# Kernel optimization log

Hardware: AMD Instinct MI355X
Metric: run time of the kernel (lower is better)

The kernel has to match this reference:

```python
import jax, jax.numpy as jnp
import numpy as np

H = 128        # num_hidden
NIN = 384      # num_in
FF = 4 * H
SCALE = 30.0
EPS = 1e-5


def _gelu(x):
    return jax.nn.gelu(x, approximate=False)


def _layernorm(x, g, b):
    mu = jnp.mean(x, axis=-1, keepdims=True)
    var = jnp.var(x, axis=-1, keepdims=True)
    return (x - mu) * jax.lax.rsqrt(var + EPS) * g + b


def setup_inputs() -> dict:
    key = jax.random.key(0)
    ks = jax.random.split(key, 12)
    B, N, K = 4, 2048, 48
    s = lambda fan_in: 1.0 / np.sqrt(fan_in)
    inp = {
        "h_V": jax.random.normal(ks[0], (B, N, H), jnp.float32),
        "h_E": jax.random.normal(ks[1], (B, N, K, NIN), jnp.float32),
        "mask_V": jnp.ones((B, N), jnp.float32),
        "mask_attend": jnp.ones((B, N, K), jnp.float32),
        "W1_w": jax.random.uniform(ks[2], (H + NIN, H), jnp.float32, -s(H + NIN), s(H + NIN)),
        "W1_b": jnp.zeros((H,), jnp.float32),
        "W2_w": jax.random.uniform(ks[3], (H, H), jnp.float32, -s(H), s(H)),
        "W2_b": jnp.zeros((H,), jnp.float32),
        "W3_w": jax.random.uniform(ks[4], (H, H), jnp.float32, -s(H), s(H)),
        "W3_b": jnp.zeros((H,), jnp.float32),
        "Win_w": jax.random.uniform(ks[5], (H, FF), jnp.float32, -s(H), s(H)),
        "Win_b": jnp.zeros((FF,), jnp.float32),
        "Wout_w": jax.random.uniform(ks[6], (FF, H), jnp.float32, -s(FF), s(FF)),
        "Wout_b": jnp.zeros((H,), jnp.float32),
        "ln1_g": jnp.ones((H,), jnp.float32),
        "ln1_b": jnp.zeros((H,), jnp.float32),
        "ln2_g": jnp.ones((H,), jnp.float32),
        "ln2_b": jnp.zeros((H,), jnp.float32),
    }
    return inp


def reference(h_V, h_E, mask_V, mask_attend,
              W1_w, W1_b, W2_w, W2_b, W3_w, W3_b,
              Win_w, Win_b, Wout_w, Wout_b,
              ln1_g, ln1_b, ln2_g, ln2_b):
    B, N, K, _ = h_E.shape
    # expand node feats over K neighbors and concat with edge feats -> [B,N,K,H+NIN]
    h_V_expand = jnp.broadcast_to(h_V[:, :, None, :], (B, N, K, h_V.shape[-1]))
    h_EV = jnp.concatenate([h_V_expand, h_E], axis=-1)
    # edge MLP: 3 linears, 2 GELUs
    h_message = _gelu(h_EV @ W1_w + W1_b)
    h_message = _gelu(h_message @ W2_w + W2_b)
    h_message = h_message @ W3_w + W3_b
    h_message = mask_attend[..., None] * h_message
    dh = jnp.sum(h_message, axis=-2) / SCALE  # [B,N,H]
    h = _layernorm(h_V + dh, ln1_g, ln1_b)
    # position-wise FFN
    dh = _gelu(h @ Win_w + Win_b) @ Wout_w + Wout_b
    h = _layernorm(h + dh, ln2_g, ln2_b)
    h = mask_V[..., None] * h
    return h
```

## Files before the change

kernel.cpp:

```cpp
#include <hip/hip_runtime.h>
#include <hip/hip_bf16.h>

#define Hh    128
#define NINc  384
#define KN    48
#define FFd   512
#define NNODE 8192

typedef __attribute__((ext_vector_type(8))) short short8v;
typedef __attribute__((ext_vector_type(4))) float f32x4;

__device__ __forceinline__ short f2bf1(float f){
  union { __hip_bfloat16 h; short s; } c; c.h = __float2bfloat16(f);
  return c.s;
}
__device__ __forceinline__ unsigned pk_bf16(float lo, float hi){
  union { __hip_bfloat162 h; unsigned u; } c;
  c.h = __float22bfloat162_rn(make_float2(lo, hi));
  return c.u;
}

__device__ __forceinline__ float gelu_f(float x){
  float t = 0.7978845608028654f * x * (1.0f + 0.044715f * x * x);
  float e = __expf(2.0f * t);
  return x * (1.0f - 1.0f / (e + 1.0f));
}

__device__ __forceinline__ void bar_lds(){
  asm volatile("s_waitcnt lgkmcnt(0)\n\ts_barrier" ::: "memory");
}

__global__ void prep_weights(const float* __restrict__ W1, const float* __restrict__ W2,
                             const float* __restrict__ W3, const float* __restrict__ Win,
                             const float* __restrict__ Wout,
                             short* __restrict__ w1vT, short* __restrict__ w1p,
                             short* __restrict__ w2p,  short* __restrict__ w3p,
                             short* __restrict__ winT, short* __restrict__ woutT)
{
  int i = blockIdx.x * 256 + threadIdx.x;
  if (i < 16384){ int n = i / 128, k = i % 128; w1vT[i] = f2bf1(W1[k*128 + n]); return; }
  i -= 16384;
  if (i < 49152){
    int n = i / 6144, r = i % 6144;
    int ks = r / 512, r2 = r % 512;
    int lane = r2 / 8, j = r2 % 8;
    int qq = lane >> 4, arow = lane & 15;
    w1p[i] = f2bf1(W1[(128 + ks*32 + qq*8 + j)*128 + n*16 + arow]); return;
  }
  i -= 49152;
  if (i < 16384){
    int n = i / 2048, r = i % 2048;
    int ks = r / 512, r2 = r % 512;
    int lane = r2 / 8, j = r2 % 8;
    int qq = lane >> 4, arow = lane & 15;
    w2p[i] = f2bf1(W2[(ks*32 + qq*8 + j)*128 + n*16 + arow]); return;
  }
  i -= 16384;
  if (i < 16384){
    int n = i / 2048, r = i % 2048;
    int ks = r / 512, r2 = r % 512;
    int lane = r2 / 8, j = r2 % 8;
    int qq = lane >> 4, arow = lane & 15;
    w3p[i] = f2bf1(W3[(ks*32 + qq*8 + j)*128 + n*16 + arow]); return;
  }
  i -= 16384;
  if (i < 65536){ int n = i / 128, k = i % 128; winT[i] = f2bf1(Win[k*512 + n]); return; }
  i -= 65536;
  if (i < 65536){ int n = i / 512, k = i % 512; woutT[i] = f2bf1(Wout[k*128 + n]); return; }
}

__global__ __launch_bounds__(256,2) void np_kernel(
    const float* __restrict__ hV, const short* __restrict__ w1vT,
    const float* __restrict__ b1, float* __restrict__ npart)
{
  const int row0 = blockIdx.x * 64;
  const int tid = threadIdx.x, lane = tid & 63, wv = tid >> 6;
  __shared__ __attribute__((aligned(16))) short Xs[64][Hh + 8];

  const float4* src = (const float4*)(hV + (size_t)row0 * Hh);
  #pragma unroll
  for (int j = 0; j < 8; ++j){
    int idx = tid + 256*j;
    int r = idx >> 5, c4 = idx & 31;
    float4 v = src[idx];
    *(uint2*)&Xs[r][c4*4] = make_uint2(pk_bf16(v.x,v.y), pk_bf16(v.z,v.w));
  }
  __syncthreads();

  const int arow = lane & 15, kgrp = (lane >> 4) * 8;
  const int col0 = wv * 32, ccol = lane & 15, crow0 = (lane >> 4) * 4;

  f32x4 acc[4][2];
  #pragma unroll
  for (int m = 0; m < 4; ++m) for (int n = 0; n < 2; ++n) acc[m][n] = (f32x4){0.f,0.f,0.f,0.f};

  const short8v* Bw = (const short8v*)w1vT;
  #pragma unroll
  for (int ks = 0; ks < 4; ++ks){
    int kb = ks*32 + kgrp;
    short8v b0 = Bw[(col0 + arow)*16      + (kb >> 3)];
    short8v b1f = Bw[(col0 + 16 + arow)*16 + (kb >> 3)];
    #pragma unroll
    for (int m = 0; m < 4; ++m){
      short8v a = *(const short8v*)&Xs[m*16 + arow][kb];
      acc[m][0] = __builtin_amdgcn_mfma_f32_16x16x32_bf16(a, b0,  acc[m][0], 0,0,0);
      acc[m][1] = __builtin_amdgcn_mfma_f32_16x16x32_bf16(a, b1f, acc[m][1], 0,0,0);
    }
  }
  #pragma unroll
  for (int m = 0; m < 4; ++m) for (int n = 0; n < 2; ++n){
    int colg = col0 + n*16 + ccol;
    float bb = b1[colg];
    #pragma unroll
    for (int r = 0; r < 4; ++r)
      npart[(size_t)(row0 + m*16 + crow0 + r)*Hh + colg] = acc[m][n][r] + bb;
  }
}

__global__ __launch_bounds__(256,3) void edge_kernel(
    const float* __restrict__ hE, const float* __restrict__ hV,
    const float* __restrict__ maskA, const float* __restrict__ npart,
    const short* __restrict__ w1p, const short* __restrict__ w2p,
    const short* __restrict__ w3p,
    const float* __restrict__ b2, const float* __restrict__ b3,
    float* __restrict__ out)
{
  const int node = blockIdx.x;
  const int tid = threadIdx.x, lane = tid & 63, wv = tid >> 6;
  const int e = lane & 15, q = lane >> 4, kgrp = q * 8;
  const int n0 = wv * 32;

  __shared__ __attribute__((aligned(16))) short Et[KN][NINc + 8];
  __shared__ __attribute__((aligned(16))) short M1[KN][136];
  short (*M2)[136] = (short (*)[136])&Et[0][0];

  {
    const float4* src = (const float4*)(hE + (size_t)node * (KN*NINc));
    #pragma unroll
    for (int h = 0; h < 2; ++h){
      float4 pf[9];
      #pragma unroll
      for (int j = 0; j < 9; ++j) pf[j] = src[tid + 256*(9*h + j)];
      #pragma unroll
      for (int j = 0; j < 9; ++j){
        int idx = tid + 256*(9*h + j);
        int r = idx / 96, c4 = idx - r*96;
        *(uint2*)&Et[r][c4*4] = make_uint2(pk_bf16(pf[j].x, pf[j].y),
                                           pk_bf16(pf[j].z, pf[j].w));
      }
    }
  }

  const float4 npv0 = *(const float4*)(npart + (size_t)node*Hh + n0 + 4*q);
  const float4 npv1 = *(const float4*)(npart + (size_t)node*Hh + n0 + 16 + 4*q);
  const float4 b2v0 = *(const float4*)(b2 + n0 + 4*q);
  const float4 b2v1 = *(const float4*)(b2 + n0 + 16 + 4*q);
  const float4 b3v0 = *(const float4*)(b3 + n0 + 4*q);
  const float4 b3v1 = *(const float4*)(b3 + n0 + 16 + 4*q);
  const float4 hvv0 = *(const float4*)(hV + (size_t)node*Hh + n0 + 4*q);
  const float4 hvv1 = *(const float4*)(hV + (size_t)node*Hh + n0 + 16 + 4*q);
  const float mk0 = maskA[node*KN + e];
  const float mk1 = maskA[node*KN + 16 + e];
  const float mk2 = maskA[node*KN + 32 + e];

  __syncthreads();

  const f32x4 Z = (f32x4){0.f,0.f,0.f,0.f};

  {
    f32x4 a00=Z, a10=Z, a20=Z, a01=Z, a11=Z, a21=Z;
    const short8v* B1 = (const short8v*)w1p;
    #pragma unroll
    for (int ks = 0; ks < 12; ++ks){
      short8v f0 = B1[((2*wv  )*12 + ks)*64 + lane];
      short8v f1 = B1[((2*wv+1)*12 + ks)*64 + lane];
      int kb = ks*32 + kgrp;
      short8v t0 = *(const short8v*)&Et[e][kb];
      short8v t1 = *(const short8v*)&Et[16 + e][kb];
      short8v t2 = *(const short8v*)&Et[32 + e][kb];
      a00 = __builtin_amdgcn_mfma_f32_16x16x32_bf16(f0, t0, a00, 0,0,0);
      a10 = __builtin_amdgcn_mfma_f32_16x16x32_bf16(f0, t1, a10, 0,0,0);
      a20 = __builtin_amdgcn_mfma_f32_16x16x32_bf16(f0, t2, a20, 0,0,0);
      a01 = __builtin_amdgcn_mfma_f32_16x16x32_bf16(f1, t0, a01, 0,0,0);
      a11 = __builtin_amdgcn_mfma_f32_16x16x32_bf16(f1, t1, a11, 0,0,0);
      a21 = __builtin_amdgcn_mfma_f32_16x16x32_bf16(f1, t2, a21, 0,0,0);
    }
    #define WR_M(DST, ACC, ET, COLB, BV)  { short4 s;                 \
      s.x = f2bf1(gelu_f(ACC[0] + BV.x));                             \
      s.y = f2bf1(gelu_f(ACC[1] + BV.y));                             \
      s.z = f2bf1(gelu_f(ACC[2] + BV.z));                             \
      s.w = f2bf1(gelu_f(ACC[3] + BV.w));                             \
      *(short4*)&DST[16*ET + e][COLB + 4*q] = s; }
    WR_M(M1, a00, 0, n0,      npv0)  WR_M(M1, a10, 1, n0,      npv0)
    WR_M(M1, a20, 2, n0,      npv0)  WR_M(M1, a01, 0, n0 + 16, npv1)
    WR_M(M1, a11, 1, n0 + 16, npv1)  WR_M(M1, a21, 2, n0 + 16, npv1)
  }
  bar_lds();

  {
    f32x4 c00=Z, c10=Z, c20=Z, c01=Z, c11=Z, c21=Z;
    const short8v* B2f = (const short8v*)w2p;
    #pragma unroll
    for (int ks = 0; ks < 4; ++ks){
      short8v f0 = B2f[((2*wv  )*4 + ks)*64 + lane];
      short8v f1 = B2f[((2*wv+1)*4 + ks)*64 + lane];
      int kb = ks*32 + kgrp;
      short8v t0 = *(const short8v*)&M1[e][kb];
      short8v t1 = *(const short8v*)&M1[16 + e][kb];
      short8v t2 = *(const short8v*)&M1[32 + e][kb];
      c00 = __builtin_amdgcn_mfma_f32_16x16x32_bf16(f0, t0, c00, 0,0,0);
      c10 = __builtin_amdgcn_mfma_f32_16x16x32_bf16(f0, t1, c10, 0,0,0);
      c20 = __builtin_amdgcn_mfma_f32_16x16x32_bf16(f0, t2, c20, 0,0,0);
      c01 = __builtin_amdgcn_mfma_f32_16x16x32_bf16(f1, t0, c01, 0,0,0);
      c11 = __builtin_amdgcn_mfma_f32_16x16x32_bf16(f1, t1, c11, 0,0,0);
      c21 = __builtin_amdgcn_mfma_f32_16x16x32_bf16(f1, t2, c21, 0,0,0);
    }
    WR_M(M2, c00, 0, n0,      b2v0)  WR_M(M2, c10, 1, n0,      b2v0)
    WR_M(M2, c20, 2, n0,      b2v0)  WR_M(M2, c01, 0, n0 + 16, b2v1)
    WR_M(M2, c11, 1, n0 + 16, b2v1)  WR_M(M2, c21, 2, n0 + 16, b2v1)
  }
  bar_lds();

  {
    f32x4 d00=Z, d10=Z, d20=Z, d01=Z, d11=Z, d21=Z;
    const short8v* B3f = (const short8v*)w3p;
    #pragma unroll
    for (int ks = 0; ks < 4; ++ks){
      short8v f0 = B3f[((2*wv  )*4 + ks)*64 + lane];
      short8v f1 = B3f[((2*wv+1)*4 + ks)*64 + lane];
      int kb = ks*32 + kgrp;
      short8v t0 = *(const short8v*)&M2[e][kb];
      short8v t1 = *(const short8v*)&M2[16 + e][kb];
      short8v t2 = *(const short8v*)&M2[32 + e][kb];
      d00 = __builtin_amdgcn_mfma_f32_16x16x32_bf16(f0, t0, d00, 0,0,0);
      d10 = __builtin_amdgcn_mfma_f32_16x16x32_bf16(f0, t1, d10, 0,0,0);
      d20 = __builtin_amdgcn_mfma_f32_16x16x32_bf16(f0, t2, d20, 0,0,0);
      d01 = __builtin_amdgcn_mfma_f32_16x16x32_bf16(f1, t0, d01, 0,0,0);
      d11 = __builtin_amdgcn_mfma_f32_16x16x32_bf16(f1, t1, d11, 0,0,0);
      d21 = __builtin_amdgcn_mfma_f32_16x16x32_bf16(f1, t2, d21, 0,0,0);
    }
    f32x4 v0, v1;
    #pragma unroll
    for (int r = 0; r < 4; ++r){
      v0[r] = (d00[r] + b3v0[r])*mk0 + (d10[r] + b3v0[r])*mk1 + (d20[r] + b3v0[r])*mk2;
      v1[r] = (d01[r] + b3v1[r])*mk0 + (d11[r] + b3v1[r])*mk1 + (d21[r] + b3v1[r])*mk2;
    }
    #pragma unroll
    for (int s = 1; s <= 8; s <<= 1){
      #pragma unroll
      for (int r = 0; r < 4; ++r){
        v0[r] += __shfl_xor(v0[r], s);
        v1[r] += __shfl_xor(v1[r], s);
      }
    }
    if (e == 0){
      float4 o0, o1;
      o0.x = hvv0.x + v0[0]*(1.0f/30.0f); o0.y = hvv0.y + v0[1]*(1.0f/30.0f);
      o0.z = hvv0.z + v0[2]*(1.0f/30.0f); o0.w = hvv0.w + v0[3]*(1.0f/30.0f);
      o1.x = hvv1.x + v1[0]*(1.0f/30.0f); o1.y = hvv1.y + v1[1]*(1.0f/30.0f);
      o1.z = hvv1.z + v1[2]*(1.0f/30.0f); o1.w = hvv1.w + v1[3]*(1.0f/30.0f);
      *(float4*)(out + (size_t)node*Hh + n0 + 4*q)      = o0;
      *(float4*)(out + (size_t)node*Hh + n0 + 16 + 4*q) = o1;
    }
  }
  #undef WR_M
}

__global__ __launch_bounds__(256,2) void ffn_kernel(
    const float* __restrict__ ln1g, const float* __restrict__ ln1b,
    const short* __restrict__ winT, const float* __restrict__ bin,
    const short* __restrict__ woutT, const float* __restrict__ bout,
    const float* __restrict__ ln2g, const float* __restrict__ ln2b,
    const float* __restrict__ maskV, float* __restrict__ io)
{
  const int row0 = blockIdx.x * 32;
  const int tid = threadIdx.x, lane = tid & 63, wv = tid >> 6;
  __shared__ __attribute__((aligned(16))) short Xs[32][Hh + 8];
  __shared__ __attribute__((aligned(16))) float Rs[32][Hh + 4];
  __shared__ __attribute__((aligned(16))) short Hs[32][FFd + 8];

  const int arow = lane & 15, kgrp = (lane >> 4) * 8;
  const int ccol = lane & 15, crow0 = (lane >> 4) * 4;

  {
    int r = tid >> 3, cb = (tid & 7) * 16;
    const float4* xp = (const float4*)(io + (size_t)(row0 + r)*Hh + cb);
    float xv[16];
    #pragma unroll
    for (int j = 0; j < 4; ++j){
      float4 v = xp[j];
      xv[j*4+0]=v.x; xv[j*4+1]=v.y; xv[j*4+2]=v.z; xv[j*4+3]=v.w;
    }
    float sum = 0.f, sq = 0.f;
    #pragma unroll
    for (int j = 0; j < 16; ++j){ sum += xv[j]; sq += xv[j]*xv[j]; }
    #pragma unroll
    for (int d = 1; d < 8; d <<= 1){ sum += __shfl_xor(sum, d); sq += __shfl_xor(sq, d); }
    float mu = sum * (1.0f/128.0f);
    float var = sq * (1.0f/128.0f) - mu*mu;
    float rstd = rsqrtf(var + 1e-5f);
    #pragma unroll
    for (int j = 0; j < 16; ++j){
      int c = cb + j;
      float xn = (xv[j] - mu) * rstd * ln1g[c] + ln1b[c];
      Xs[r][c] = f2bf1(xn);
      Rs[r][c] = xn;
    }
  }
  __syncthreads();

  {
    f32x4 acc[2][8];
    #pragma unroll
    for (int m = 0; m < 2; ++m) for (int n = 0; n < 8; ++n) acc[m][n] = (f32x4){0.f,0.f,0.f,0.f};
    const short8v* Bw = (const short8v*)winT;
    #pragma unroll
    for (int ks = 0; ks < 4; ++ks){
      int kb = ks*32 + kgrp;
      short8v a0 = *(const short8v*)&Xs[arow][kb];
      short8v a1 = *(const short8v*)&Xs[16 + arow][kb];
      #pragma unroll
      for (int n = 0; n < 8; ++n){
        short8v b = Bw[(wv*128 + n*16 + arow)*16 + (kb >> 3)];
        acc[0][n] = __builtin_amdgcn_mfma_f32_16x16x32_bf16(a0,b,acc[0][n],0,0,0);
        acc[1][n] = __builtin_amdgcn_mfma_f32_16x16x32_bf16(a1,b,acc[1][n],0,0,0);
      }
    }
    #pragma unroll
    for (int m = 0; m < 2; ++m) for (int n = 0; n < 8; ++n){
      int colg = wv*128 + n*16 + ccol;
      float bb = bin[colg];
      #pragma unroll
      for (int r = 0; r < 4; ++r)
        Hs[m*16 + crow0 + r][colg] = f2bf1(gelu_f(acc[m][n][r] + bb));
    }
  }
  __syncthreads();

  {
    f32x4 acc[2][2];
    #pragma unroll
    for (int m = 0; m < 2; ++m) for (int n = 0; n < 2; ++n) acc[m][n] = (f32x4){0.f,0.f,0.f,0.f};
    const short8v* Bw = (const short8v*)woutT;
    #pragma unroll
    for (int ks = 0; ks < 16; ++ks){
      int kb = ks*32 + kgrp;
      short8v a0 = *(const short8v*)&Hs[arow][kb];
      short8v a1 = *(const short8v*)&Hs[16 + arow][kb];
      short8v b0 = Bw[(wv*32 + arow)*64      + (kb >> 3)];
      short8v b1f = Bw[(wv*32 + 16 + arow)*64 + (kb >> 3)];
      acc[0][0] = __builtin_amdgcn_mfma_f32_16x16x32_bf16(a0,b0, acc[0][0],0,0,0);
      acc[1][0] = __builtin_amdgcn_mfma_f32_16x16x32_bf16(a1,b0, acc[1][0],0,0,0);
      acc[0][1] = __builtin_amdgcn_mfma_f32_16x16x32_bf16(a0,b1f,acc[0][1],0,0,0);
      acc[1][1] = __builtin_amdgcn_mfma_f32_16x16x32_bf16(a1,b1f,acc[1][1],0,0,0);
    }
    #pragma unroll
    for (int m = 0; m < 2; ++m) for (int n = 0; n < 2; ++n){
      int colg = wv*32 + n*16 + ccol;
      float bb = bout[colg];
      #pragma unroll
      for (int r = 0; r < 4; ++r){
        int rr = m*16 + crow0 + r;
        Rs[rr][colg] = Rs[rr][colg] + acc[m][n][r] + bb;
      }
    }
  }
  __syncthreads();

  {
    int r = tid >> 3, cb = (tid & 7) * 16;
    float xv[16];
    #pragma unroll
    for (int j = 0; j < 16; ++j) xv[j] = Rs[r][cb + j];
    float sum = 0.f, sq = 0.f;
    #pragma unroll
    for (int j = 0; j < 16; ++j){ sum += xv[j]; sq += xv[j]*xv[j]; }
    #pragma unroll
    for (int d = 1; d < 8; d <<= 1){ sum += __shfl_xor(sum, d); sq += __shfl_xor(sq, d); }
    float mu = sum * (1.0f/128.0f);
    float var = sq * (1.0f/128.0f) - mu*mu;
    float rstd = rsqrtf(var + 1e-5f);
    float mv = maskV[row0 + r];
    float* op = io + (size_t)(row0 + r)*Hh + cb;
    #pragma unroll
    for (int j = 0; j < 4; ++j){
      float4 o;
      o.x = ((xv[j*4+0] - mu)*rstd*ln2g[cb+j*4+0] + ln2b[cb+j*4+0]) * mv;
      o.y = ((xv[j*4+1] - mu)*rstd*ln2g[cb+j*4+1] + ln2b[cb+j*4+1]) * mv;
      o.z = ((xv[j*4+2] - mu)*rstd*ln2g[cb+j*4+2] + ln2b[cb+j*4+2]) * mv;
      o.w = ((xv[j*4+3] - mu)*rstd*ln2g[cb+j*4+3] + ln2b[cb+j*4+3]) * mv;
      ((float4*)op)[j] = o;
    }
  }
}

extern "C" void kernel_launch(void* const* d_in, const int* in_sizes, int n_in,
                              void* d_out, int out_size, void* d_ws, size_t ws_size,
                              hipStream_t stream)
{
  const float* hV    = (const float*)d_in[0];
  const float* hE    = (const float*)d_in[1];
  const float* maskV = (const float*)d_in[2];
  const float* maskA = (const float*)d_in[3];
  const float* W1w   = (const float*)d_in[4];
  const float* W1b   = (const float*)d_in[5];
  const float* W2w   = (const float*)d_in[6];
  const float* W2b   = (const float*)d_in[7];
  const float* W3w   = (const float*)d_in[8];
  const float* W3b   = (const float*)d_in[9];
  const float* Winw  = (const float*)d_in[10];
  const float* Winb  = (const float*)d_in[11];
  const float* Woutw = (const float*)d_in[12];
  const float* Woutb = (const float*)d_in[13];
  const float* l1g   = (const float*)d_in[14];
  const float* l1b   = (const float*)d_in[15];
  const float* l2g   = (const float*)d_in[16];
  const float* l2b   = (const float*)d_in[17];

  char* ws = (char*)d_ws;
  size_t off = 0;
  float* npart = (float*)(ws + off); off += (size_t)NNODE * Hh * 4;
  short* w1vT  = (short*)(ws + off); off += 16384*2;
  short* w1p   = (short*)(ws + off); off += 49152*2;
  short* w2p   = (short*)(ws + off); off += 16384*2;
  short* w3p   = (short*)(ws + off); off += 16384*2;
  short* winT  = (short*)(ws + off); off += 65536*2;
  short* woutT = (short*)(ws + off); off += 65536*2;
  if (ws_size < off) return;

  prep_weights<<<896, 256, 0, stream>>>(W1w, W2w, W3w, Winw, Woutw,
                                        w1vT, w1p, w2p, w3p, winT, woutT);
  np_kernel<<<NNODE/64, 256, 0, stream>>>(hV, w1vT, W1b, npart);
  edge_kernel<<<NNODE, 256, 0, stream>>>(hE, hV, maskA, npart,
                                         w1p, w2p, w3p, W2b, W3b, (float*)d_out);
  ffn_kernel<<<NNODE/32, 256, 0, stream>>>(l1g, l1b, winT, Winb, woutT, Woutb,
                                           l2g, l2b, maskV, (float*)d_out);
}
```

Baseline: 212.9 us.

## Stream edge features directly from global into MFMA operands, drop LDS staging

After: 365.8 us. 71.8% more time.

```diff
diff --git a/kernel.cpp b/kernel.cpp
--- a/kernel.cpp
+++ b/kernel.cpp
@@ -19,6 +19,12 @@
   c.h = __float22bfloat162_rn(make_float2(lo, hi));
   return c.u;
 }
+__device__ __forceinline__ short8v pack8(float4 a, float4 b){
+  union { short8v s; unsigned u[4]; } r;
+  r.u[0] = pk_bf16(a.x, a.y); r.u[1] = pk_bf16(a.z, a.w);
+  r.u[2] = pk_bf16(b.x, b.y); r.u[3] = pk_bf16(b.z, b.w);
+  return r.s;
+}
 
 __device__ __forceinline__ float gelu_f(float x){
   float t = 0.7978845608028654f * x * (1.0f + 0.044715f * x * x);
@@ -28,6 +34,13 @@
 
 __device__ __forceinline__ void bar_lds(){
   asm volatile("s_waitcnt lgkmcnt(0)\n\ts_barrier" ::: "memory");
+}
+
+__device__ __forceinline__ short* ldsAddr(short* base, int row, int colShort){
+  int raw  = colShort * 2;
+  int slot = raw >> 4, off = raw & 15;
+  int pslot = (slot & 8) | ((slot ^ row) & 7);
+  return (short*)((char*)base + row*256 + pslot*16 + off);
 }
 
 __global__ void prep_weights(const float* __restrict__ W1, const float* __restrict__ W2,
@@ -117,7 +130,7 @@
   }
 }
 
-__global__ __launch_bounds__(256,3) void edge_kernel(
+__global__ __launch_bounds__(256,4) void edge_kernel(
     const float* __restrict__ hE, const float* __restrict__ hV,
     const float* __restrict__ maskA, const float* __restrict__ npart,
     const short* __restrict__ w1p, const short* __restrict__ w2p,
@@ -127,29 +140,11 @@
 {
   const int node = blockIdx.x;
   const int tid = threadIdx.x, lane = tid & 63, wv = tid >> 6;
-  const int e = lane & 15, q = lane >> 4, kgrp = q * 8;
+  const int e = lane & 15, q = lane >> 4;
   const int n0 = wv * 32;
 
-  __shared__ __attribute__((aligned(16))) short Et[KN][NINc + 8];
-  __shared__ __attribute__((aligned(16))) short M1[KN][136];
-  short (*M2)[136] = (short (*)[136])&Et[0][0];
-
-  {
-    const float4* src = (const float4*)(hE + (size_t)node * (KN*NINc));
-    #pragma unroll
-    for (int h = 0; h < 2; ++h){
-      float4 pf[9];
-      #pragma unroll
-      for (int j = 0; j < 9; ++j) pf[j] = src[tid + 256*(9*h + j)];
-      #pragma unroll
-      for (int j = 0; j < 9; ++j){
-        int idx = tid + 256*(9*h + j);
-        int r = idx / 96, c4 = idx - r*96;
-        *(uint2*)&Et[r][c4*4] = make_uint2(pk_bf16(pf[j].x, pf[j].y),
-                                           pk_bf16(pf[j].z, pf[j].w));
-      }
-    }
-  }
+  __shared__ __attribute__((aligned(16))) short M1[KN * 128];
+  __shared__ __attribute__((aligned(16))) short M2[KN * 128];
 
   const float4 npv0 = *(const float4*)(npart + (size_t)node*Hh + n0 + 4*q);
   const float4 npv1 = *(const float4*)(npart + (size_t)node*Hh + n0 + 16 + 4*q);
@@ -163,9 +158,18 @@
   const float mk1 = maskA[node*KN + 16 + e];
   const float mk2 = maskA[node*KN + 32 + e];
 
-  __syncthreads();
-
   const f32x4 Z = (f32x4){0.f,0.f,0.f,0.f};
+  const float* eb = hE + (size_t)node * (KN*NINc);
+  const float* er0 = eb + (size_t)e        * NINc + q*8;
+  const float* er1 = eb + (size_t)(16 + e) * NINc + q*8;
+  const float* er2 = eb + (size_t)(32 + e) * NINc + q*8;
+
+  #define WR_M(DST, ACC, ET, COLB, BV)  { short4 s;                 \
+    s.x = f2bf1(gelu_f(ACC[0] + BV.x));                             \
+    s.y = f2bf1(gelu_f(ACC[1] + BV.y));                             \
+    s.z = f2bf1(gelu_f(ACC[2] + BV.z));                             \
+    s.w = f2bf1(gelu_f(ACC[3] + BV.w));                             \
+    *(short4*)ldsAddr(DST, 16*ET + e, COLB + 4*q) = s; }
 
   {
     f32x4 a00=Z, a10=Z, a20=Z, a01=Z, a11=Z, a21=Z;
@@ -174,10 +178,15 @@
     for (int ks = 0; ks < 12; ++ks){
       short8v f0 = B1[((2*wv  )*12 + ks)*64 + lane];
       short8v f1 = B1[((2*wv+1)*12 + ks)*64 + lane];
-      int kb = ks*32 + kgrp;
-      short8v t0 = *(const short8v*)&Et[e][kb];
-      short8v t1 = *(const short8v*)&Et[16 + e][kb];
-      short8v t2 = *(const short8v*)&Et[32 + e][kb];
+      float4 x0a = *(const float4*)(er0 + ks*32);
+      float4 x0b = *(const float4*)(er0 + ks*32 + 4);
+      float4 x1a = *(const float4*)(er1 + ks*32);
+      float4 x1b = *(const float4*)(er1 + ks*32 + 4);
+      float4 x2a = *(const float4*)(er2 + ks*32);
+      float4 x2b = *(const float4*)(er2 + ks*32 + 4);
+      short8v t0 = pack8(x0a, x0b);
+      short8v t1 = pack8(x1a, x1b);
+      short8v t2 = pack8(x2a, x2b);
       a00 = __builtin_amdgcn_mfma_f32_16x16x32_bf16(f0, t0, a00, 0,0,0);
       a10 = __builtin_amdgcn_mfma_f32_16x16x32_bf16(f0, t1, a10, 0,0,0);
       a20 = __builtin_amdgcn_mfma_f32_16x16x32_bf16(f0, t2, a20, 0,0,0);
@@ -185,12 +194,6 @@
       a11 = __builtin_amdgcn_mfma_f32_16x16x32_bf16(f1, t1, a11, 0,0,0);
       a21 = __builtin_amdgcn_mfma_f32_16x16x32_bf16(f1, t2, a21, 0,0,0);
     }
-    #define WR_M(DST, ACC, ET, COLB, BV)  { short4 s;                 \
-      s.x = f2bf1(gelu_f(ACC[0] + BV.x));                             \
-      s.y = f2bf1(gelu_f(ACC[1] + BV.y));                             \
-      s.z = f2bf1(gelu_f(ACC[2] + BV.z));                             \
-      s.w = f2bf1(gelu_f(ACC[3] + BV.w));                             \
-      *(short4*)&DST[16*ET + e][COLB + 4*q] = s; }
     WR_M(M1, a00, 0, n0,      npv0)  WR_M(M1, a10, 1, n0,      npv0)
     WR_M(M1, a20, 2, n0,      npv0)  WR_M(M1, a01, 0, n0 + 16, npv1)
     WR_M(M1, a11, 1, n0 + 16, npv1)  WR_M(M1, a21, 2, n0 + 16, npv1)
@@ -204,10 +207,10 @@
     for (int ks = 0; ks < 4; ++ks){
       short8v f0 = B2f[((2*wv  )*4 + ks)*64 + lane];
       short8v f1 = B2f[((2*wv+1)*4 + ks)*64 + lane];
-      int kb = ks*32 + kgrp;
-      short8v t0 = *(const short8v*)&M1[e][kb];
-      short8v t1 = *(const short8v*)&M1[16 + e][kb];
-      short8v t2 = *(const short8v*)&M1[32 + e][kb];
+      int kc = ks*32 + q*8;
+      short8v t0 = *(const short8v*)ldsAddr(M1, e,      kc);
+      short8v t1 = *(const short8v*)ldsAddr(M1, 16 + e, kc);
+      short8v t2 = *(const short8v*)ldsAddr(M1, 32 + e, kc);
       c00 = __builtin_amdgcn_mfma_f32_16x16x32_bf16(f0, t0, c00, 0,0,0);
       c10 = __builtin_amdgcn_mfma_f32_16x16x32_bf16(f0, t1, c10, 0,0,0);
       c20 = __builtin_amdgcn_mfma_f32_16x16x32_bf16(f0, t2, c20, 0,0,0);
@@ -228,10 +231,10 @@
     for (int ks = 0; ks < 4; ++ks){
       short8v f0 = B3f[((2*wv  )*4 + ks)*64 + lane];
       short8v f1 = B3f[((2*wv+1)*4 + ks)*64 + lane];
-      int kb = ks*32 + kgrp;
-      short8v t0 = *(const short8v*)&M2[e][kb];
-      short8v t1 = *(const short8v*)&M2[16 + e][kb];
-      short8v t2 = *(const short8v*)&M2[32 + e][kb];
+      int kc = ks*32 + q*8;
+      short8v t0 = *(const short8v*)ldsAddr(M2, e,      kc);
+      short8v t1 = *(const short8v*)ldsAddr(M2, 16 + e, kc);
+      short8v t2 = *(const short8v*)ldsAddr(M2, 32 + e, kc);
       d00 = __builtin_amdgcn_mfma_f32_16x16x32_bf16(f0, t0, d00, 0,0,0);
       d10 = __builtin_amdgcn_mfma_f32_16x16x32_bf16(f0, t1, d10, 0,0,0);
       d20 = __builtin_amdgcn_mfma_f32_16x16x32_bf16(f0, t2, d20, 0,0,0);
```

## Split each node's neighbors across two blocks and add combine kernel

Applied to the files above, without the earlier changes.

Result: slower. 241.4 us (+13.4%).

```diff
diff --git a/kernel.cpp b/kernel.cpp
--- a/kernel.cpp
+++ b/kernel.cpp
@@ -117,37 +117,46 @@
   }
 }
 
-__global__ __launch_bounds__(256,3) void edge_kernel(
-    const float* __restrict__ hE, const float* __restrict__ hV,
+__global__ __launch_bounds__(256,4) void edge_kernel(
+    const float* __restrict__ hE,
     const float* __restrict__ maskA, const float* __restrict__ npart,
     const short* __restrict__ w1p, const short* __restrict__ w2p,
     const short* __restrict__ w3p,
     const float* __restrict__ b2, const float* __restrict__ b3,
-    float* __restrict__ out)
-{
-  const int node = blockIdx.x;
+    float* __restrict__ pbuf)
+{
+  const int bid  = blockIdx.x;
+  const int node = bid >> 1, half = bid & 1;
   const int tid = threadIdx.x, lane = tid & 63, wv = tid >> 6;
-  const int e = lane & 15, q = lane >> 4, kgrp = q * 8;
+  const int e = lane & 15, q = lane >> 4;
   const int n0 = wv * 32;
 
-  __shared__ __attribute__((aligned(16))) short Et[KN][NINc + 8];
-  __shared__ __attribute__((aligned(16))) short M1[KN][136];
+  __shared__ __attribute__((aligned(16))) short Et[32][NINc + 8];
+  __shared__ __attribute__((aligned(16))) short M1[32][136];
   short (*M2)[136] = (short (*)[136])&Et[0][0];
 
   {
-    const float4* src = (const float4*)(hE + (size_t)node * (KN*NINc));
-    #pragma unroll
-    for (int h = 0; h < 2; ++h){
-      float4 pf[9];
-      #pragma unroll
-      for (int j = 0; j < 9; ++j) pf[j] = src[tid + 256*(9*h + j)];
-      #pragma unroll
-      for (int j = 0; j < 9; ++j){
-        int idx = tid + 256*(9*h + j);
-        int r = idx / 96, c4 = idx - r*96;
-        *(uint2*)&Et[r][c4*4] = make_uint2(pk_bf16(pf[j].x, pf[j].y),
-                                           pk_bf16(pf[j].z, pf[j].w));
-      }
+    unsigned* zp = (unsigned*)&Et[24][0];
+    #pragma unroll
+    for (int z = 0; z < 7; ++z) zp[tid + 256*z] = 0;
+    if (tid < 1568 - 1792 + 256) {}
+  }
+  {
+    unsigned* zp = (unsigned*)&Et[24][0];
+    for (int z = tid; z < 1568; z += 256) zp[z] = 0;
+  }
+
+  {
+    const float4* src = (const float4*)(hE + ((size_t)node*KN + half*24) * NINc);
+    float4 pf[9];
+    #pragma unroll
+    for (int j = 0; j < 9; ++j) pf[j] = src[tid + 256*j];
+    #pragma unroll
+    for (int j = 0; j < 9; ++j){
+      int idx = tid + 256*j;
+      int r = idx / 96, c4 = idx - r*96;
+      *(uint2*)&Et[r][c4*4] = make_uint2(pk_bf16(pf[j].x, pf[j].y),
+                                         pk_bf16(pf[j].z, pf[j].w));
     }
   }
 
@@ -157,93 +166,80 @@
   const float4 b2v1 = *(const float4*)(b2 + n0 + 16 + 4*q);
   const float4 b3v0 = *(const float4*)(b3 + n0 + 4*q);
   const float4 b3v1 = *(const float4*)(b3 + n0 + 16 + 4*q);
-  const float4 hvv0 = *(const float4*)(hV + (size_t)node*Hh + n0 + 4*q);
-  const float4 hvv1 = *(const float4*)(hV + (size_t)node*Hh + n0 + 16 + 4*q);
-  const float mk0 = maskA[node*KN + e];
-  const float mk1 = maskA[node*KN + 16 + e];
-  const float mk2 = maskA[node*KN + 32 + e];
+  const float mk0 = maskA[node*KN + half*24 + e];
+  const float mk1 = (e < 8) ? maskA[node*KN + half*24 + 16 + e] : 0.f;
 
   __syncthreads();
 
   const f32x4 Z = (f32x4){0.f,0.f,0.f,0.f};
 
-  {
-    f32x4 a00=Z, a10=Z, a20=Z, a01=Z, a11=Z, a21=Z;
+  #define WR_M(DST, ACC, ET, COLB, BV)  { short4 s;                 \
+    s.x = f2bf1(gelu_f(ACC[0] + BV.x));                             \
+    s.y = f2bf1(gelu_f(ACC[1] + BV.y));                             \
+    s.z = f2bf1(gelu_f(ACC[2] + BV.z));                             \
+    s.w = f2bf1(gelu_f(ACC[3] + BV.w));                             \
+    *(short4*)&DST[16*ET + e][COLB + 4*q] = s; }
+
+  {
+    f32x4 a00=Z, a10=Z, a01=Z, a11=Z;
     const short8v* B1 = (const short8v*)w1p;
     #pragma unroll
     for (int ks = 0; ks < 12; ++ks){
       short8v f0 = B1[((2*wv  )*12 + ks)*64 + lane];
       short8v f1 = B1[((2*wv+1)*12 + ks)*64 + lane];
-      int kb = ks*32 + kgrp;
+      int kb = ks*32 + q*8;
       short8v t0 = *(const short8v*)&Et[e][kb];
       short8v t1 = *(const short8v*)&Et[16 + e][kb];
-      short8v t2 = *(const short8v*)&Et[32 + e][kb];
       a00 = __builtin_amdgcn_mfma_f32_16x16x32_bf16(f0, t0, a00, 0,0,0);
       a10 = __builtin_amdgcn_mfma_f32_16x16x32_bf16(f0, t1, a10, 0,0,0);
-      a20 = __builtin_amdgcn_mfma_f32_16x16x32_bf16(f0, t2, a20, 0,0,0);
       a01 = __builtin_amdgcn_mfma_f32_16x16x32_bf16(f1, t0, a01, 0,0,0);
       a11 = __builtin_amdgcn_mfma_f32_16x16x32_bf16(f1, t1, a11, 0,0,0);
-      a21 = __builtin_amdgcn_mfma_f32_16x16x32_bf16(f1, t2, a21, 0,0,0);
-    }
-    #define WR_M(DST, ACC, ET, COLB, BV)  { short4 s;                 \
-      s.x = f2bf1(gelu_f(ACC[0] + BV.x));                             \
-      s.y = f2bf1(gelu_f(ACC[1] + BV.y));                             \
-      s.z = f2bf1(gelu_f(ACC[2] + BV.z));                             \
-      s.w = f2bf1(gelu_f(ACC[3] + BV.w));                             \
-      *(short4*)&DST[16*ET + e][COLB + 4*q] = s; }
+    }
     WR_M(M1, a00, 0, n0,      npv0)  WR_M(M1, a10, 1, n0,      npv0)
-    WR_M(M1, a20, 2, n0,      npv0)  WR_M(M1, a01, 0, n0 + 16, npv1)
-    WR_M(M1, a11, 1, n0 + 16, npv1)  WR_M(M1, a21, 2, n0 + 16, npv1)
+    WR_M(M1, a01, 0, n0 + 16, npv1)  WR_M(M1, a11, 1, n0 + 16, npv1)
   }
   bar_lds();
 
   {
-    f32x4 c00=Z, c10=Z, c20=Z, c01=Z, c11=Z, c21=Z;
+    f32x4 c00=Z, c10=Z, c01=Z, c11=Z;
     const short8v* B2f = (const short8v*)w2p;
     #pragma unroll
     for (int ks = 0; ks < 4; ++ks){
       short8v f0 = B2f[((2*wv  )*4 + ks)*64 + lane];
       short8v f1 = B2f[((2*wv+1)*4 + ks)*64 + lane];
-      int kb = ks*32 + kgrp;
+      int kb = ks*32 + q*8;
       short8v t0 = *(const short8v*)&M1[e][kb];
       short8v t1 = *(const short8v*)&M1[16 + e][kb];
-      short8v t2 = *(const short8v*)&M1[32 + e][kb];
       c00 = __builtin_amdgcn_mfma_f32_16x16x32_bf16(f0, t0, c00, 0,0,0);
       c10 = __builtin_amdgcn_mfma_f32_16x16x32_bf16(f0, t1, c10, 0,0,0);
-      c20 = __builtin_amdgcn_mfma_f32_16x16x32_bf16(f0, t2, c20, 0,0,0);
       c01 = __builtin_amdgcn_mfma_f32_16x16x32_bf16(f1, t0, c01, 0,0,0);
       c11 = __builtin_amdgcn_mfma_f32_16x16x32_bf16(f1, t1, c11, 0,0,0);
-      c21 = __builtin_amdgcn_mfma_f32_16x16x32_bf16(f1, t2, c21, 0,0,0);
     }
     WR_M(M2, c00, 0, n0,      b2v0)  WR_M(M2, c10, 1, n0,      b2v0)
-    WR_M(M2, c20, 2, n0,      b2v0)  WR_M(M2, c01, 0, n0 + 16, b2v1)
-    WR_M(M2, c11, 1, n0 + 16, b2v1)  WR_M(M2, c21, 2, n0 + 16, b2v1)
+    WR_M(M2, c01, 0, n0 + 16, b2v1)  WR_M(M2, c11, 1, n0 + 16, b2v1)
   }
   bar_lds();
 
   {
-    f32x4 d00=Z, d10=Z, d20=Z, d01=Z, d11=Z, d21=Z;
+    f32x4 d00=Z, d10=Z, d01=Z, d11=Z;
     const short8v* B3f = (const short8v*)w3p;
     #pragma unroll
     for (int ks = 0; ks < 4; ++ks){
       short8v f0 = B3f[((2*wv  )*4 + ks)*64 + lane];
       short8v f1 = B3f[((2*wv+1)*4 + ks)*64 + lane];
-      int kb = ks*32 + kgrp;
+      int kb = ks*32 + q*8;
       short8v t0 = *(const short8v*)&M2[e][kb];
       short8v t1 = *(const short8v*)&M2[16 + e][kb];
-      short8v t2 = *(const short8v*)&M2[32 + e][kb];
       d00 = __builtin_amdgcn_mfma_f32_16x16x32_bf16(f0, t0, d00, 0,0,0);
       d10 = __builtin_amdgcn_mfma_f32_16x16x32_bf16(f0, t1, d10, 0,0,0);
-      d20 = __builtin_amdgcn_mfma_f32_16x16x32_bf16(f0, t2, d20, 0,0,0);
       d01 = __builtin_amdgcn_mfma_f32_16x16x32_bf16(f1, t0, d01, 0,0,0);
       d11 = __builtin_amdgcn_mfma_f32_16x16x32_bf16(f1, t1, d11, 0,0,0);
-      d21 = __builtin_amdgcn_mfma_f32_16x16x32_bf16(f1, t2, d21, 0,0,0);
     }
     f32x4 v0, v1;
     #pragma unroll
     for (int r = 0; r < 4; ++r){
-      v0[r] = (d00[r] + b3v0[r])*mk0 + (d10[r] + b3v0[r])*mk1 + (d20[r] + b3v0[r])*mk2;
-      v1[r] = (d01[r] + b3v1[r])*mk0 + (d11[r] + b3v1[r])*mk1 + (d21[r] + b3v1[r])*mk2;
+      v0[r] = (d00[r] + b3v0[r])*mk0 + (d10[r] + b3v0[r])*mk1;
+      v1[r] = (d01[r] + b3v1[r])*mk0 + (d11[r] + b3v1[r])*mk1;
     }
     #pragma unroll
     for (int s = 1; s <= 8; s <<= 1){
@@ -255,15 +251,30 @@
     }
     if (e == 0){
       float4 o0, o1;
-      o0.x = hvv0.x + v0[0]*(1.0f/30.0f); o0.y = hvv0.y + v0[1]*(1.0f/30.0f);
-      o0.z = hvv0.z + v0[2]*(1.0f/30.0f); o0.w = hvv0.w + v0[3]*(1.0f/30.0f);
-      o1.x = hvv1.x + v1[0]*(1.0f/30.0f); o1.y = hvv1.y + v1[1]*(1.0f/30.0f);
-      o1.z = hvv1.z + v1[2]*(1.0f/30.0f); o1.w = hvv1.w + v1[3]*(1.0f/30.0f);
-      *(float4*)(out + (size_t)node*Hh + n0 + 4*q)      = o0;
-      *(float4*)(out + (size_t)node*Hh + n0 + 16 + 4*q) = o1;
+      o0.x = v0[0]; o0.y = v0[1]; o0.z = v0[2]; o0.w = v0[3];
+      o1.x = v1[0]; o1.y = v1[1]; o1.z = v1[2]; o1.w = v1[3];
+      *(float4*)(pbuf + (size_t)bid*Hh + n0 + 4*q)      = o0;
+      *(float4*)(pbuf + (size_t)bid*Hh + n0 + 16 + 4*q) = o1;
     }
   }
   #undef WR_M
+}
+
+__global__ __launch_bounds__(256,8) void combine_kernel(
+    const float* __restrict__ hV, const float* __restrict__ pbuf,
+    float* __restrict__ out)
+{
+  int gid = blockIdx.x * 256 + threadIdx.x;
+  int node = gid >> 5, c4 = gid & 31;
+  float4 a = *(const float4*)(pbuf + ((size_t)(2*node)    )*Hh + c4*4);
+  float4 b = *(const float4*)(pbuf + ((size_t)(2*node) + 1)*Hh + c4*4);
+  float4 h = *(const float4*)(hV + (size_t)node*Hh + c4*4);
+  float4 o;
+  o.x = h.x + (a.x + b.x)*(1.0f/30.0f);
+  o.y = h.y + (a.y + b.y)*(1.0f/30.0f);
+  o.z = h.z + (a.z + b.z)*(1.0f/30.0f);
+  o.w = h.w + (a.w + b.w)*(1.0f/30.0f);
+  *(float4*)(out + (size_t)node*Hh + c4*4) = o;
 }
 
 __global__ __launch_bounds__(256,2) void ffn_kernel(
@@ -420,6 +431,7 @@
   char* ws = (char*)d_ws;
   size_t off = 0;
   float* npart = (float*)(ws + off); off += (size_t)NNODE * Hh * 4;
+  float* pbuf  = (float*)(ws + off); off += (size_t)NNODE * 2 * Hh * 4;
   short* w1vT  = (short*)(ws + off); off += 16384*2;
   short* w1p   = (short*)(ws + off); off += 49152*2;
   short* w2p   = (short*)(ws + off); off += 16384*2;
@@ -431,8 +443,9 @@
   prep_weights<<<896, 256, 0, stream>>>(W1w, W2w, W3w, Winw, Woutw,
                                         w1vT, w1p, w2p, w3p, winT, woutT);
   np_kernel<<<NNODE/64, 256, 0, stream>>>(hV, w1vT, W1b, npart);
-  edge_kernel<<<NNODE, 256, 0, stream>>>(hE, hV, maskA, npart,
-                                         w1p, w2p, w3p, W2b, W3b, (float*)d_out);
+  edge_kernel<<<NNODE*2, 256, 0, stream>>>(hE, maskA, npart,
+                                           w1p, w2p, w3p, W2b, W3b, pbuf);
+  combine_kernel<<<NNODE*Hh/4/256, 256, 0, stream>>>(hV, pbuf, (float*)d_out);
   ffn_kernel<<<NNODE/32, 256, 0, stream>>>(l1g, l1b, winT, Winb, woutT, Woutb,
                                            l2g, l2b, maskV, (float*)d_out);
 }
```

## Alias edge MLP scratch buffers into the edge tile to raise occupancy

Applied to the files above, without the earlier changes.

New measurement: 204.7 us. 1.04x faster.

```diff
diff --git a/kernel.cpp b/kernel.cpp
--- a/kernel.cpp
+++ b/kernel.cpp
@@ -69,17 +69,17 @@
   if (i < 65536){ int n = i / 512, k = i % 512; woutT[i] = f2bf1(Wout[k*128 + n]); return; }
 }
 
-__global__ __launch_bounds__(256,2) void np_kernel(
+__global__ __launch_bounds__(256,4) void np_kernel(
     const float* __restrict__ hV, const short* __restrict__ w1vT,
     const float* __restrict__ b1, float* __restrict__ npart)
 {
-  const int row0 = blockIdx.x * 64;
+  const int row0 = blockIdx.x * 32;
   const int tid = threadIdx.x, lane = tid & 63, wv = tid >> 6;
-  __shared__ __attribute__((aligned(16))) short Xs[64][Hh + 8];
+  __shared__ __attribute__((aligned(16))) short Xs[32][Hh + 8];
 
   const float4* src = (const float4*)(hV + (size_t)row0 * Hh);
   #pragma unroll
-  for (int j = 0; j < 8; ++j){
+  for (int j = 0; j < 4; ++j){
     int idx = tid + 256*j;
     int r = idx >> 5, c4 = idx & 31;
     float4 v = src[idx];
@@ -90,9 +90,9 @@
   const int arow = lane & 15, kgrp = (lane >> 4) * 8;
   const int col0 = wv * 32, ccol = lane & 15, crow0 = (lane >> 4) * 4;
 
-  f32x4 acc[4][2];
+  f32x4 acc[2][2];
   #pragma unroll
-  for (int m = 0; m < 4; ++m) for (int n = 0; n < 2; ++n) acc[m][n] = (f32x4){0.f,0.f,0.f,0.f};
+  for (int m = 0; m < 2; ++m) for (int n = 0; n < 2; ++n) acc[m][n] = (f32x4){0.f,0.f,0.f,0.f};
 
   const short8v* Bw = (const short8v*)w1vT;
   #pragma unroll
@@ -101,14 +101,14 @@
     short8v b0 = Bw[(col0 + arow)*16      + (kb >> 3)];
     short8v b1f = Bw[(col0 + 16 + arow)*16 + (kb >> 3)];
     #pragma unroll
-    for (int m = 0; m < 4; ++m){
+    for (int m = 0; m < 2; ++m){
       short8v a = *(const short8v*)&Xs[m*16 + arow][kb];
       acc[m][0] = __builtin_amdgcn_mfma_f32_16x16x32_bf16(a, b0,  acc[m][0], 0,0,0);
       acc[m][1] = __builtin_amdgcn_mfma_f32_16x16x32_bf16(a, b1f, acc[m][1], 0,0,0);
     }
   }
   #pragma unroll
-  for (int m = 0; m < 4; ++m) for (int n = 0; n < 2; ++n){
+  for (int m = 0; m < 2; ++m) for (int n = 0; n < 2; ++n){
     int colg = col0 + n*16 + ccol;
     float bb = b1[colg];
     #pragma unroll
@@ -117,7 +117,7 @@
   }
 }
 
-__global__ __launch_bounds__(256,3) void edge_kernel(
+__global__ __launch_bounds__(256,4) void edge_kernel(
     const float* __restrict__ hE, const float* __restrict__ hV,
     const float* __restrict__ maskA, const float* __restrict__ npart,
     const short* __restrict__ w1p, const short* __restrict__ w2p,
@@ -127,54 +127,59 @@
 {
   const int node = blockIdx.x;
   const int tid = threadIdx.x, lane = tid & 63, wv = tid >> 6;
-  const int e = lane & 15, q = lane >> 4, kgrp = q * 8;
+  const int e = lane & 15, q = lane >> 4;
   const int n0 = wv * 32;
 
   __shared__ __attribute__((aligned(16))) short Et[KN][NINc + 8];
-  __shared__ __attribute__((aligned(16))) short M1[KN][136];
-  short (*M2)[136] = (short (*)[136])&Et[0][0];
+  short (*M1)[136] = (short (*)[136])&Et[0][0];
+  short (*M2)[136] = (short (*)[136])(&Et[0][0] + KN*136);
 
   {
     const float4* src = (const float4*)(hE + (size_t)node * (KN*NINc));
-    #pragma unroll
-    for (int h = 0; h < 2; ++h){
-      float4 pf[9];
-      #pragma unroll
-      for (int j = 0; j < 9; ++j) pf[j] = src[tid + 256*(9*h + j)];
-      #pragma unroll
-      for (int j = 0; j < 9; ++j){
-        int idx = tid + 256*(9*h + j);
-        int r = idx / 96, c4 = idx - r*96;
-        *(uint2*)&Et[r][c4*4] = make_uint2(pk_bf16(pf[j].x, pf[j].y),
-                                           pk_bf16(pf[j].z, pf[j].w));
-      }
+    float4 pfa[9], pfb[9];
+    #pragma unroll
+    for (int j = 0; j < 9; ++j){
+      pfa[j] = src[2*tid     + 512*j];
+      pfb[j] = src[2*tid + 1 + 512*j];
+    }
+    #pragma unroll
+    for (int j = 0; j < 9; ++j){
+      int idx = 2*tid + 512*j;
+      int r = idx / 96, c = idx - r*96;
+      uint4 u;
+      u.x = pk_bf16(pfa[j].x, pfa[j].y);
+      u.y = pk_bf16(pfa[j].z, pfa[j].w);
+      u.z = pk_bf16(pfb[j].x, pfb[j].y);
+      u.w = pk_bf16(pfb[j].z, pfb[j].w);
+      *(uint4*)&Et[r][c*4] = u;
     }
   }
 
   const float4 npv0 = *(const float4*)(npart + (size_t)node*Hh + n0 + 4*q);
   const float4 npv1 = *(const float4*)(npart + (size_t)node*Hh + n0 + 16 + 4*q);
-  const float4 b2v0 = *(const float4*)(b2 + n0 + 4*q);
-  const float4 b2v1 = *(const float4*)(b2 + n0 + 16 + 4*q);
-  const float4 b3v0 = *(const float4*)(b3 + n0 + 4*q);
-  const float4 b3v1 = *(const float4*)(b3 + n0 + 16 + 4*q);
-  const float4 hvv0 = *(const float4*)(hV + (size_t)node*Hh + n0 + 4*q);
-  const float4 hvv1 = *(const float4*)(hV + (size_t)node*Hh + n0 + 16 + 4*q);
   const float mk0 = maskA[node*KN + e];
   const float mk1 = maskA[node*KN + 16 + e];
   const float mk2 = maskA[node*KN + 32 + e];
 
-  __syncthreads();
+  bar_lds();
 
   const f32x4 Z = (f32x4){0.f,0.f,0.f,0.f};
 
-  {
-    f32x4 a00=Z, a10=Z, a20=Z, a01=Z, a11=Z, a21=Z;
+  #define WR_M(DST, ACC, ET, COLB, BV)  { short4 s;                 \
+    s.x = f2bf1(gelu_f(ACC[0] + BV.x));                             \
+    s.y = f2bf1(gelu_f(ACC[1] + BV.y));                             \
+    s.z = f2bf1(gelu_f(ACC[2] + BV.z));                             \
+    s.w = f2bf1(gelu_f(ACC[3] + BV.w));                             \
+    *(short4*)&DST[16*ET + e][COLB + 4*q] = s; }
+
+  f32x4 a00=Z, a10=Z, a20=Z, a01=Z, a11=Z, a21=Z;
+  {
     const short8v* B1 = (const short8v*)w1p;
     #pragma unroll
     for (int ks = 0; ks < 12; ++ks){
       short8v f0 = B1[((2*wv  )*12 + ks)*64 + lane];
       short8v f1 = B1[((2*wv+1)*12 + ks)*64 + lane];
-      int kb = ks*32 + kgrp;
+      int kb = ks*32 + q*8;
       short8v t0 = *(const short8v*)&Et[e][kb];
       short8v t1 = *(const short8v*)&Et[16 + e][kb];
       short8v t2 = *(const short8v*)&Et[32 + e][kb];
@@ -185,12 +190,13 @@
       a11 = __builtin_amdgcn_mfma_f32_16x16x32_bf16(f1, t1, a11, 0,0,0);
       a21 = __builtin_amdgcn_mfma_f32_16x16x32_bf16(f1, t2, a21, 0,0,0);
     }
-    #define WR_M(DST, ACC, ET, COLB, BV)  { short4 s;                 \
-      s.x = f2bf1(gelu_f(ACC[0] + BV.x));                             \
-      s.y = f2bf1(gelu_f(ACC[1] + BV.y));                             \
-      s.z = f2bf1(gelu_f(ACC[2] + BV.z));                             \
-      s.w = f2bf1(gelu_f(ACC[3] + BV.w));                             \
-      *(short4*)&DST[16*ET + e][COLB + 4*q] = s; }
+  }
+  bar_lds();
+
+  const float4 b2v0 = *(const float4*)(b2 + n0 + 4*q);
+  const float4 b2v1 = *(const float4*)(b2 + n0 + 16 + 4*q);
+
+  {
     WR_M(M1, a00, 0, n0,      npv0)  WR_M(M1, a10, 1, n0,      npv0)
     WR_M(M1, a20, 2, n0,      npv0)  WR_M(M1, a01, 0, n0 + 16, npv1)
     WR_M(M1, a11, 1, n0 + 16, npv1)  WR_M(M1, a21, 2, n0 + 16, npv1)
@@ -204,7 +210,7 @@
     for (int ks = 0; ks < 4; ++ks){
       short8v f0 = B2f[((2*wv  )*4 + ks)*64 + lane];
       short8v f1 = B2f[((2*wv+1)*4 + ks)*64 + lane];
-      int kb = ks*32 + kgrp;
+      int kb = ks*32 + q*8;
       short8v t0 = *(const short8v*)&M1[e][kb];
       short8v t1 = *(const short8v*)&M1[16 + e][kb];
       short8v t2 = *(const short8v*)&M1[32 + e][kb];
@@ -219,6 +225,12 @@
     WR_M(M2, c20, 2, n0,      b2v0)  WR_M(M2, c01, 0, n0 + 16, b2v1)
     WR_M(M2, c11, 1, n0 + 16, b2v1)  WR_M(M2, c21, 2, n0 + 16, b2v1)
   }
+
+  const float4 b3v0 = *(const float4*)(b3 + n0 + 4*q);
+  const float4 b3v1 = *(const float4*)(b3 + n0 + 16 + 4*q);
+  const float4 hvv0 = *(const float4*)(hV + (size_t)node*Hh + n0 + 4*q);
+  const float4 hvv1 = *(const float4*)(hV + (size_t)node*Hh + n0 + 16 + 4*q);
+
   bar_lds();
 
   {
@@ -228,7 +240,7 @@
     for (int ks = 0; ks < 4; ++ks){
       short8v f0 = B3f[((2*wv  )*4 + ks)*64 + lane];
       short8v f1 = B3f[((2*wv+1)*4 + ks)*64 + lane];
-      int kb = ks*32 + kgrp;
+      int kb = ks*32 + q*8;
       short8v t0 = *(const short8v*)&M2[e][kb];
       short8v t1 = *(const short8v*)&M2[16 + e][kb];
       short8v t2 = *(const short8v*)&M2[32 + e][kb];
@@ -430,7 +442,7 @@
 
   prep_weights<<<896, 256, 0, stream>>>(W1w, W2w, W3w, Winw, Woutw,
                                         w1vT, w1p, w2p, w3p, winT, woutT);
-  np_kernel<<<NNODE/64, 256, 0, stream>>>(hV, w1vT, W1b, npart);
+  np_kernel<<<NNODE/32, 256, 0, stream>>>(hV, w1vT, W1b, npart);
   edge_kernel<<<NNODE, 256, 0, stream>>>(hE, hV, maskA, npart,
                                          w1p, w2p, w3p, W2b, W3b, (float*)d_out);
   ffn_kernel<<<NNODE/32, 256, 0, stream>>>(l1g, l1b, winT, Winb, woutT, Woutb,
```
